# Performance work log

Measured on AMD Instinct MI355X. Metric: run time of the kernel, lower is better.

## Reference

```python
import jax, jax.numpy as jnp
import numpy as np

B, T, S, H = 32, 512, 1024, 1024

def setup_inputs() -> dict:
    key = jax.random.key(0)
    k1, k2, k3, k4, k5, k6 = jax.random.split(key, 6)
    query = jax.random.normal(k1, (B, T, H), dtype=jnp.float32)
    encoder_outputs = jax.random.normal(k2, (B, S, H), dtype=jnp.float32)
    # lengths in [S//2, S], force max length == S so mask width matches score
    src_lengths = jax.random.randint(k3, (B,), S // 2, S + 1, dtype=jnp.int32)
    src_lengths = src_lengths.at[0].set(S).astype(jnp.int64)
    scale = 1.0 / np.sqrt(H)
    W_in = jax.random.normal(k4, (H, H), dtype=jnp.float32) * scale      # linear_in.weight
    W_out = jax.random.normal(k5, (H, 2 * H), dtype=jnp.float32) * scale # linear_out.weight
    b_out = jax.random.normal(k6, (H,), dtype=jnp.float32) * scale       # linear_out.bias
    return {"query": query, "encoder_outputs": encoder_outputs,
            "src_lengths": src_lengths, "W_in": W_in, "W_out": W_out, "b_out": b_out}

def reference(query, encoder_outputs, src_lengths, W_in, W_out, b_out):
    # padding mask: True where position >= length  [B, S]
    pad = jnp.arange(S)[None, :] >= src_lengths[:, None]
    # linear_in (no bias): [B, T, H]
    qw = jnp.einsum('bth,oh->bto', query, W_in)
    # scores: [B, T, S]
    score = jnp.einsum('bto,bso->bts', qw, encoder_outputs)
    score = jnp.where(pad[:, None, :], -jnp.inf, score)
    p = jax.nn.softmax(score, axis=2)
    # context: [B, T, H]
    c = jnp.einsum('bts,bsh->bth', p, encoder_outputs)
    concat = jnp.concatenate([query, c], axis=2)          # [B, T, 2H]
    out = jnp.tanh(jnp.einsum('btk,ok->bto', concat, W_out) + b_out)
    return out
```

## Files before the change

kernel.cpp:

```cpp
#include <hip/hip_runtime.h>
#include <math.h>

#define BB 32
#define TT 512
#define SS 1024
#define HH 1024

typedef __attribute__((ext_vector_type(8))) short short8;
typedef __attribute__((ext_vector_type(4))) float f32x4;
typedef __attribute__((ext_vector_type(4))) unsigned short u16x4;
typedef unsigned short u16;
typedef unsigned int u32;

__device__ __forceinline__ u16 f2h(float x) {
    union { float f; unsigned int u; } a; a.f = x;
    unsigned int u = a.u;
    return (u16)((u + 0x7fffu + ((u >> 16) & 1u)) >> 16);
}
__device__ __forceinline__ float h2f(u16 h) {
    union { unsigned int u; float f; } a; a.u = ((unsigned int)h) << 16;
    return a.f;
}

__device__ __forceinline__ void gll16(const u16* g, u16* l) {
    __builtin_amdgcn_global_load_lds(
        (const __attribute__((address_space(1))) void*)g,
        (__attribute__((address_space(3))) void*)l, 16, 0, 0);
}

enum { E_F32 = 0, E_SPLIT = 1, E_TANH = 2, E_H = 3 };

struct Segs { const u16* a[4]; const u16* b[4]; };

template<int NSEG, int EPI>
__global__ __launch_bounds__(512, 2) void gemm8(
    Segs sg, int ldA, int ldB, int zshift,
    long sA, long sB, long sC,
    const float* __restrict__ bias,
    float* __restrict__ Cf, u16* __restrict__ Ch, u16* __restrict__ Cl,
    int ldC)
{
    __shared__ u16 lds[2][2][2][256 * 32];

    const int tid = threadIdx.x;
    const int l = tid & 63, w = tid >> 6;
    const int wr = w >> 2, wc = w & 3;
    const int fr = l & 15, g = l >> 4;

    const int id = blockIdx.x;
    const int v = ((id & 7) << 5) | (id >> 3);
    const int z = v >> zshift;
    const int rest = v & ((1 << zshift) - 1);
    const int bm = (rest >> 2) * 256;
    const int bn = (rest & 3) * 256;

    const u16* Aseg[4]; const u16* Bseg[4];
#pragma unroll
    for (int s = 0; s < NSEG; ++s) {
        Aseg[s] = sg.a[s] + (long)z * sA;
        Bseg[s] = sg.b[s] + (long)z * sB;
    }
    if (EPI == E_F32 || EPI == E_TANH) Cf += (long)z * sC;
    else { Ch += (long)z * sC; if (EPI == E_SPLIT) Cl += (long)z * sC; }

    f32x4 acc[8][4] = {};

    const int srow = tid >> 2, sch = tid & 3;
    const int skc = sch ^ ((srow >> 1) & 3);
    const long grA0 = (long)(bm + srow) * ldA + skc * 8;
    const long grA1 = (long)(bm + 128 + srow) * ldA + skc * 8;
    const long grB0 = (long)(bn + srow) * ldB + skc * 8;
    const long grB1 = (long)(bn + 128 + srow) * ldB + skc * 8;
    const int ldst0 = (tid & ~63) * 8;
    const int ldst1 = (512 + (tid & ~63)) * 8;

    auto stage = [&](int tile, int kh, int tensor) {
        const int k0g = tile * 64 + kh * 32;
        const int seg = k0g >> 10, kl = k0g & 1023;
        u16* lb = &lds[tile & 1][tensor][kh][0];
        if (tensor) {
            const u16* b = Bseg[seg];
            gll16(b + grB0 + kl, lb + ldst0);
            gll16(b + grB1 + kl, lb + ldst1);
        } else {
            const u16* a = Aseg[seg];
            gll16(a + grA0 + kl, lb + ldst0);
            gll16(a + grA1 + kl, lb + ldst1);
        }
    };

    int offA[8], offB[4];
#pragma unroll
    for (int k = 0; k < 8; ++k) {
        const int r = wr * 128 + k * 16 + fr;
        offA[k] = (r * 4 + (g ^ ((r >> 1) & 3))) * 8;
    }
#pragma unroll
    for (int j = 0; j < 4; ++j) {
        const int r = wc * 64 + j * 16 + fr;
        offB[j] = (r * 4 + (g ^ ((r >> 1) & 3))) * 8;
    }

    short8 faX[4], faY[4], fbA[4], fbB[4];

#define PFA(FA, BUF, KS, MH)                                                   \
    { const u16* pl = &lds[BUF][0][KS][0];                                     \
      _Pragma("unroll") for (int i_ = 0; i_ < 4; ++i_)                         \
          FA[i_] = *(const short8*)&pl[offA[(MH) * 4 + i_]]; }
#define PFB(FB, BUF, KS)                                                       \
    { const u16* pl = &lds[BUF][1][KS][0];                                     \
      _Pragma("unroll") for (int j_ = 0; j_ < 4; ++j_)                         \
          FB[j_] = *(const short8*)&pl[offB[j_]]; }
#define MFMA16(FA, FB, MH)                                                     \
    __builtin_amdgcn_s_setprio(1);                                             \
    _Pragma("unroll") for (int i_ = 0; i_ < 4; ++i_)                           \
        _Pragma("unroll") for (int j_ = 0; j_ < 4; ++j_)                       \
            acc[(MH) * 4 + i_][j_] = __builtin_amdgcn_mfma_f32_16x16x32_bf16(  \
                FA[i_], FB[j_], acc[(MH) * 4 + i_][j_], 0, 0, 0);              \
    __builtin_amdgcn_s_setprio(0);

    stage(0, 0, 0); stage(0, 0, 1); stage(0, 1, 0); stage(0, 1, 1);
    asm volatile("s_waitcnt vmcnt(0)" ::: "memory");
    __builtin_amdgcn_s_barrier();
    PFB(fbA, 0, 0)
    PFA(faX, 0, 0, 0)
    __builtin_amdgcn_sched_barrier(0);

    const int NT = NSEG * 16;
    for (int t = 0; t < NT; ++t) {
        const int cur = t & 1, nxt = cur ^ 1;
        const bool nl = (t + 1 < NT);

        if (nl) stage(t + 1, 0, 0);
        __builtin_amdgcn_s_barrier();
        PFA(faY, cur, 0, 1)
        __builtin_amdgcn_sched_barrier(0);
        MFMA16(faX, fbA, 0)

        if (nl) stage(t + 1, 0, 1);
        if (nl) { asm volatile("s_waitcnt vmcnt(4)" ::: "memory"); }
        else    { asm volatile("s_waitcnt vmcnt(0)" ::: "memory"); }
        __builtin_amdgcn_s_barrier();
        PFB(fbB, cur, 1)
        PFA(faX, cur, 1, 0)
        __builtin_amdgcn_sched_barrier(0);
        MFMA16(faY, fbA, 1)

        if (nl) stage(t + 1, 1, 0);
        __builtin_amdgcn_s_barrier();
        PFA(faY, cur, 1, 1)
        __builtin_amdgcn_sched_barrier(0);
        MFMA16(faX, fbB, 0)

        if (nl) stage(t + 1, 1, 1);
        if (nl) { asm volatile("s_waitcnt vmcnt(4)" ::: "memory"); }
        __builtin_amdgcn_s_barrier();
        PFB(fbA, nxt, 0)
        PFA(faX, nxt, 0, 0)
        __builtin_amdgcn_sched_barrier(0);
        MFMA16(faY, fbB, 1)
    }
#undef PFA
#undef PFB
#undef MFMA16

    __syncthreads();
    const int lrow = wr * 16 + g * 4;
#pragma unroll
    for (int mi = 0; mi < 8; ++mi) {
        if (EPI == E_F32 || EPI == E_TANH) {
            float* el = (float*)&lds[0][0][0][0];
#pragma unroll
            for (int nj = 0; nj < 4; ++nj) {
                const int col = wc * 64 + nj * 16 + fr;
                const float bv = (EPI == E_TANH) ? bias[bn + col] : 0.0f;
#pragma unroll
                for (int r = 0; r < 4; ++r) {
                    float vv = acc[mi][nj][r];
                    if (EPI == E_TANH) {
                        const float e = __expf(2.0f * (vv + bv));
                        vv = 1.0f - 2.0f / (e + 1.0f);
                    }
                    el[(lrow + r) * 260 + col] = vv;
                }
            }
            __syncthreads();
#pragma unroll
            for (int q = 0; q < 4; ++q) {
                const int c = tid + 512 * q;
                const int r32 = c >> 6, c4 = (c & 63) * 4;
                f32x4 vv = *(const f32x4*)&el[r32 * 260 + c4];
                const int grow = bm + (r32 >> 4) * 128 + mi * 16 + (r32 & 15);
                *(f32x4*)&Cf[(long)grow * ldC + bn + c4] = vv;
            }
        } else if (EPI == E_SPLIT) {
            u32* el = (u32*)&lds[0][0][0][0];
#pragma unroll
            for (int nj = 0; nj < 4; ++nj) {
                const int col = wc * 64 + nj * 16 + fr;
#pragma unroll
                for (int r = 0; r < 4; ++r) {
                    const float vv = acc[mi][nj][r];
                    const u16 h = f2h(vv);
                    const u16 lo = f2h(vv - h2f(h));
                    el[(lrow + r) * 260 + col] = (u32)h | ((u32)lo << 16);
                }
            }
            __syncthreads();
#pragma unroll
            for (int q = 0; q < 4; ++q) {
                const int c = tid + 512 * q;
                const int r32 = c >> 6, c4 = (c & 63) * 4;
                const u32* p = &el[r32 * 260 + c4];
                u16x4 hh, ll;
#pragma unroll
                for (int e = 0; e < 4; ++e) {
                    const u32 pv = p[e];
                    hh[e] = (u16)(pv & 0xffffu);
                    ll[e] = (u16)(pv >> 16);
                }
                const int grow = bm + (r32 >> 4) * 128 + mi * 16 + (r32 & 15);
                const long o = (long)grow * ldC + bn + c4;
                *(u16x4*)&Ch[o] = hh;
                *(u16x4*)&Cl[o] = ll;
            }
        } else {
            u16* el = (u16*)&lds[0][0][0][0];
#pragma unroll
            for (int nj = 0; nj < 4; ++nj) {
                const int col = wc * 64 + nj * 16 + fr;
#pragma unroll
                for (int r = 0; r < 4; ++r)
                    el[(lrow + r) * 264 + col] = f2h(acc[mi][nj][r]);
            }
            __syncthreads();
#pragma unroll
            for (int q = 0; q < 2; ++q) {
                const int c = tid + 512 * q;
                const int r32 = c >> 5, c8 = (c & 31) * 8;
                short8 vv = *(const short8*)&el[r32 * 264 + c8];
                const int grow = bm + (r32 >> 4) * 128 + mi * 16 + (r32 & 15);
                *(short8*)&Ch[(long)grow * ldC + bn + c8] = vv;
            }
        }
        __syncthreads();
    }
}

__global__ __launch_bounds__(256) void split_f32(
    const float* __restrict__ in, u16* __restrict__ hi, u16* __restrict__ lo,
    long n4)
{
    long i = (long)blockIdx.x * blockDim.x + threadIdx.x;
    const long stride = (long)gridDim.x * blockDim.x;
    for (; i < n4; i += stride) {
        f32x4 v = *(const f32x4*)(in + i * 4);
        u16x4 h4, l4;
#pragma unroll
        for (int e = 0; e < 4; ++e) {
            u16 h_ = f2h(v[e]);
            h4[e] = h_; l4[e] = f2h(v[e] - h2f(h_));
        }
        *(u16x4*)(hi + i * 4) = h4;
        *(u16x4*)(lo + i * 4) = l4;
    }
}

__global__ __launch_bounds__(256) void split3(
    const float* __restrict__ q,  u16* __restrict__ qh,  u16* __restrict__ ql,
    const float* __restrict__ wi, u16* __restrict__ wih, u16* __restrict__ wil,
    const float* __restrict__ wo, u16* __restrict__ woh, u16* __restrict__ wol,
    long nq4, long nwi4, long nwo4)
{
    const long total = nq4 + nwi4 + nwo4;
    long i = (long)blockIdx.x * blockDim.x + threadIdx.x;
    const long stride = (long)gridDim.x * blockDim.x;
    for (; i < total; i += stride) {
        const float* src; u16 *hi, *lo; long off;
        if (i < nq4)              { src = q;  hi = qh;  lo = ql;  off = i; }
        else if (i < nq4 + nwi4)  { src = wi; hi = wih; lo = wil; off = i - nq4; }
        else                      { src = wo; hi = woh; lo = wol; off = i - nq4 - nwi4; }
        f32x4 v = *(const f32x4*)(src + off * 4);
        u16x4 h4, l4;
#pragma unroll
        for (int e = 0; e < 4; ++e) {
            u16 h_ = f2h(v[e]);
            h4[e] = h_; l4[e] = f2h(v[e] - h2f(h_));
        }
        *(u16x4*)(hi + off * 4) = h4;
        *(u16x4*)(lo + off * 4) = l4;
    }
}

__global__ __launch_bounds__(256) void split_enc_fused(
    const float* __restrict__ in, u16* __restrict__ hi, u16* __restrict__ lo,
    u16* __restrict__ outT)
{
    __shared__ u16 t[64][72];
    const int z = blockIdx.z, sb = blockIdx.x * 64, hb = blockIdx.y * 64;
    const int c4 = (threadIdx.x & 15) * 4, r0 = threadIdx.x >> 4;
    const float* src = in + ((long)z * SS + sb) * HH + hb;
    u16* dhi = hi + ((long)z * SS + sb) * HH + hb;
    u16* dlo = lo + ((long)z * SS + sb) * HH + hb;
#pragma unroll
    for (int i = 0; i < 4; ++i) {
        const int r = r0 + i * 16;
        f32x4 v = *(const f32x4*)(src + (long)r * HH + c4);
        u16x4 h4, l4;
#pragma unroll
        for (int j = 0; j < 4; ++j) {
            u16 h_ = f2h(v[j]);
            h4[j] = h_; l4[j] = f2h(v[j] - h2f(h_));
        }
        *(u16x4*)(dhi + (long)r * HH + c4) = h4;
        *(u16x4*)(dlo + (long)r * HH + c4) = l4;
        t[c4 + 0][r] = h4[0]; t[c4 + 1][r] = h4[1];
        t[c4 + 2][r] = h4[2]; t[c4 + 3][r] = h4[3];
    }
    __syncthreads();
    u16* dst = outT + ((long)z * HH + hb) * SS + sb;
#pragma unroll
    for (int i = 0; i < 4; ++i) {
        const int r = r0 + i * 16;
        u16x4 o;
#pragma unroll
        for (int j = 0; j < 4; ++j) o[j] = t[r][c4 + j];
        *(u16x4*)(dst + (long)r * SS + c4) = o;
    }
}

__global__ __launch_bounds__(256) void transpose_h(
    const u16* __restrict__ in, u16* __restrict__ out)
{
    __shared__ u16 t[64][72];
    const int z = blockIdx.z, sb = blockIdx.x * 64, hb = blockIdx.y * 64;
    const int c4 = (threadIdx.x & 15) * 4, r0 = threadIdx.x >> 4;
    const u16* src = in + ((long)z * SS + sb) * HH + hb;
#pragma unroll
    for (int i = 0; i < 4; ++i) {
        const int r = r0 + i * 16;
        u16x4 v = *(const u16x4*)(src + (long)r * HH + c4);
        t[c4 + 0][r] = v[0]; t[c4 + 1][r] = v[1];
        t[c4 + 2][r] = v[2]; t[c4 + 3][r] = v[3];
    }
    __syncthreads();
    u16* dst = out + ((long)z * HH + hb) * SS + sb;
#pragma unroll
    for (int i = 0; i < 4; ++i) {
        const int r = r0 + i * 16;
        u16x4 o;
#pragma unroll
        for (int j = 0; j < 4; ++j) o[j] = t[r][c4 + j];
        *(u16x4*)(dst + (long)r * SS + c4) = o;
    }
}

__global__ __launch_bounds__(256) void softmax_mask(
    const float* __restrict__ Sc, u16* __restrict__ Ph,
    const int* __restrict__ lens)
{
    const int row = blockIdx.x;
    const int b = row >> 9;
    const int len = lens[b];
    const float* p = Sc + (long)row * SS;

    const int tid = threadIdx.x;
    const int s0 = tid * 4;
    f32x4 v = *(const f32x4*)(p + s0);
    float vals[4] = {v.x, v.y, v.z, v.w};

    float mx = -INFINITY;
#pragma unroll
    for (int j = 0; j < 4; ++j) {
        if (s0 + j >= len) vals[j] = -INFINITY;
        mx = fmaxf(mx, vals[j]);
    }
    for (int off = 32; off; off >>= 1) mx = fmaxf(mx, __shfl_xor(mx, off, 64));

    __shared__ float redm[4];
    __shared__ float reds[4];
    const int wave = tid >> 6, lane = tid & 63;
    if (lane == 0) redm[wave] = mx;
    __syncthreads();
    mx = fmaxf(fmaxf(redm[0], redm[1]), fmaxf(redm[2], redm[3]));

    float sum = 0.0f;
#pragma unroll
    for (int j = 0; j < 4; ++j) {
        vals[j] = __expf(vals[j] - mx);
        sum += vals[j];
    }
    for (int off = 32; off; off >>= 1) sum += __shfl_xor(sum, off, 64);
    if (lane == 0) reds[wave] = sum;
    __syncthreads();
    sum = reds[0] + reds[1] + reds[2] + reds[3];

    const float inv = 1.0f / sum;
    u16x4 o;
#pragma unroll
    for (int j = 0; j < 4; ++j) o[j] = f2h(vals[j] * inv);
    *(u16x4*)(Ph + (long)row * SS + s0) = o;
}

extern "C" void kernel_launch(void* const* d_in, const int* in_sizes, int n_in,
                              void* d_out, int out_size, void* d_ws, size_t ws_size,
                              hipStream_t stream)
{
    const float* query = (const float*)d_in[0];
    const float* enc   = (const float*)d_in[1];
    const int*   lens  = (const int*)d_in[2];
    const float* W_in  = (const float*)d_in[3];
    const float* W_out = (const float*)d_in[4];
    const float* b_out = (const float*)d_in[5];
    float* out = (float*)d_out;

    const long MQ = (long)BB * TT;

    u16* qh   = (u16*)d_ws;
    u16* ql   = qh   + MQ * HH;
    u16* qwh  = ql   + MQ * HH;
    u16* qwl  = qwh  + MQ * HH;
    u16* ench = qwl  + MQ * HH;
    u16* encl = ench + (long)BB * SS * HH;
    u16* ph   = encl + (long)BB * SS * HH;
    u16* wih  = ph   + MQ * SS;
    u16* wil  = wih  + (long)HH * HH;
    u16* woh  = wil  + (long)HH * HH;
    u16* wol  = woh  + (long)HH * 2 * HH;
    float* scores = (float*)(wol + (long)HH * 2 * HH);
    u16* ch   = ql;

    u16* encT_ded = (u16*)(scores + MQ * SS);
    const size_t need_fused =
        (size_t)((u16*)(scores + MQ * SS) - (u16*)d_ws) * 2 + (size_t)BB * HH * SS * 2;
    const bool fused = (ws_size >= need_fused);
    u16* encTh = fused ? encT_ded : (u16*)scores;

    split3<<<2048, 256, 0, stream>>>(
        query, qh, ql, W_in, wih, wil, W_out, woh, wol,
        MQ * HH / 4, (long)HH * HH / 4, (long)HH * 2 * HH / 4);
    if (fused) {
        split_enc_fused<<<dim3(16, 16, 32), 256, 0, stream>>>(
            enc, ench, encl, encTh);
    } else {
        split_f32<<<2048, 256, 0, stream>>>(enc, ench, encl,
                                            (long)BB * SS * HH / 4);
    }

    Segs s1 = {{qh, qh, ql, nullptr}, {wih, wil, wih, nullptr}};
    gemm8<3, E_SPLIT><<<256, 512, 0, stream>>>(
        s1, HH, HH, 8, 0L, 0L, 0L, nullptr, nullptr, qwh, qwl, HH);

    Segs s2 = {{qwh, qwh, qwl, nullptr}, {ench, encl, ench, nullptr}};
    gemm8<3, E_F32><<<256, 512, 0, stream>>>(
        s2, HH, HH, 3, (long)TT * HH, (long)SS * HH, (long)TT * SS,
        nullptr, scores, nullptr, nullptr, SS);

    softmax_mask<<<BB * TT, 256, 0, stream>>>(scores, ph, lens);

    if (!fused) {
        transpose_h<<<dim3(16, 16, 32), 256, 0, stream>>>(ench, encTh);
    }

    Segs s3 = {{ph, nullptr, nullptr, nullptr}, {encTh, nullptr, nullptr, nullptr}};
    gemm8<1, E_H><<<256, 512, 0, stream>>>(
        s3, SS, SS, 3, (long)TT * SS, (long)HH * SS, (long)TT * HH,
        nullptr, nullptr, ch, nullptr, HH);

    Segs s4 = {{qh, ch, qh, ch},
               {woh, woh + 1024, wol, wol + 1024}};
    gemm8<4, E_TANH><<<256, 512, 0, stream>>>(
        s4, HH, 2 * HH, 8, 0L, 0L, 0L, b_out, out, nullptr, nullptr, HH);
}
```

Measured before the change: 477.3 us.

## Share hi/lo operand tiles across split-bf16 products in a fused GEMM kernel

Adds a GEMM kernel that loads each K-tile's A_hi, A_lo, B_hi and B_lo once into LDS and issues all split-precision MFMA products from them, instead of treating each product as a separate K segment. It is used for the query projection, score and output GEMMs. The intent is to cut redundant global-to-LDS traffic and loop overhead. The cost is more LDS per block and a more intricate barrier/waitcnt schedule.

```diff
diff --git a/kernel.cpp b/kernel.cpp
--- a/kernel.cpp
+++ b/kernel.cpp
@@ -31,6 +31,253 @@
 enum { E_F32 = 0, E_SPLIT = 1, E_TANH = 2, E_H = 3 };
 
 struct Segs { const u16* a[4]; const u16* b[4]; };
+
+template<int NPROD, int NKSEG, int EPI>
+__global__ __launch_bounds__(512, 2) void gemm_np(
+    const u16* __restrict__ Ah0_g, const u16* __restrict__ Ah1_g,
+    const u16* __restrict__ Al_g,
+    const u16* __restrict__ Bh_g, const u16* __restrict__ Bl_g,
+    int ldA, int ldB, int zshift,
+    long sA, long sB, long sC,
+    const float* __restrict__ bias,
+    float* __restrict__ Cf, u16* __restrict__ Ch, u16* __restrict__ Cl,
+    int ldC)
+{
+    constexpr int NTEN = (NPROD == 3) ? 4 : 3;
+    __shared__ u16 lds[2][NTEN][256 * 32];
+
+    const int tid = threadIdx.x;
+    const int l = tid & 63, w = tid >> 6;
+    const int wr = w >> 2, wc = w & 3;
+    const int fr = l & 15, g = l >> 4;
+
+    const int id = blockIdx.x;
+    const int v = ((id & 7) << 5) | (id >> 3);
+    const int z = v >> zshift;
+    const int rest = v & ((1 << zshift) - 1);
+    const int bm = (rest >> 2) * 256;
+    const int bn = (rest & 3) * 256;
+
+    const u16* Ah0 = Ah0_g + (long)z * sA;
+    const u16* Ah1 = Ah1_g;
+    const u16* Al  = (NPROD == 3) ? (Al_g + (long)z * sA) : nullptr;
+    const u16* Bh  = Bh_g + (long)z * sB;
+    const u16* Bl  = Bl_g + (long)z * sB;
+    if (EPI == E_F32 || EPI == E_TANH) Cf += (long)z * sC;
+    else { Ch += (long)z * sC; if (EPI == E_SPLIT) Cl += (long)z * sC; }
+
+    f32x4 acc[8][4] = {};
+
+    const int srow = tid >> 2, sch = tid & 3;
+    const int skc = sch ^ ((srow >> 1) & 3);
+    const long grA0 = (long)(bm + srow) * ldA + skc * 8;
+    const long grA1 = (long)(bm + 128 + srow) * ldA + skc * 8;
+    const long grB0 = (long)(bn + srow) * ldB + skc * 8;
+    const long grB1 = (long)(bn + 128 + srow) * ldB + skc * 8;
+    const int ldst0 = (tid & ~63) * 8;
+    const int ldst1 = (512 + (tid & ~63)) * 8;
+
+    auto stage = [&](int tile, int ten) {
+        const int k0g = tile * 32;
+        u16* lb = &lds[tile & 1][ten][0];
+        if (ten == 0) {
+            const u16* base = (NKSEG == 2 && k0g >= 1024) ? Ah1 : Ah0;
+            const int ka = (NKSEG == 2) ? (k0g & 1023) : k0g;
+            gll16(base + grA0 + ka, lb + ldst0);
+            gll16(base + grA1 + ka, lb + ldst1);
+        } else if (ten == 3) {
+            gll16(Al + grA0 + k0g, lb + ldst0);
+            gll16(Al + grA1 + k0g, lb + ldst1);
+        } else {
+            const u16* b = (ten == 1) ? Bh : Bl;
+            gll16(b + grB0 + k0g, lb + ldst0);
+            gll16(b + grB1 + k0g, lb + ldst1);
+        }
+    };
+
+    int offA[8], offB[4];
+#pragma unroll
+    for (int k = 0; k < 8; ++k) {
+        const int r = wr * 128 + k * 16 + fr;
+        offA[k] = (r * 4 + (g ^ ((r >> 1) & 3))) * 8;
+    }
+#pragma unroll
+    for (int j = 0; j < 4; ++j) {
+        const int r = wc * 64 + j * 16 + fr;
+        offB[j] = (r * 4 + (g ^ ((r >> 1) & 3))) * 8;
+    }
+
+    short8 fax[4], fay[4], fal[4], fbh[4], fbl[4];
+
+#define PFA_(DST, BUF, TEN, MH)                                                \
+    { const u16* pl = &lds[BUF][TEN][0];                                       \
+      _Pragma("unroll") for (int i_ = 0; i_ < 4; ++i_)                         \
+          DST[i_] = *(const short8*)&pl[offA[(MH) * 4 + i_]]; }
+#define PFB_(DST, BUF, TEN)                                                    \
+    { const u16* pl = &lds[BUF][TEN][0];                                       \
+      _Pragma("unroll") for (int j_ = 0; j_ < 4; ++j_)                         \
+          DST[j_] = *(const short8*)&pl[offB[j_]]; }
+#define MFMA16(FA, FB, MH)                                                     \
+    __builtin_amdgcn_s_setprio(1);                                             \
+    _Pragma("unroll") for (int i_ = 0; i_ < 4; ++i_)                           \
+        _Pragma("unroll") for (int j_ = 0; j_ < 4; ++j_)                       \
+            acc[(MH) * 4 + i_][j_] = __builtin_amdgcn_mfma_f32_16x16x32_bf16(  \
+                FA[i_], FB[j_], acc[(MH) * 4 + i_][j_], 0, 0, 0);              \
+    __builtin_amdgcn_s_setprio(0);
+
+    stage(0, 0); stage(0, 1); stage(0, 2);
+    if (NPROD == 3) stage(0, 3);
+    if (NPROD == 3) { asm volatile("s_waitcnt vmcnt(4)" ::: "memory"); }
+    else            { asm volatile("s_waitcnt vmcnt(2)" ::: "memory"); }
+    __builtin_amdgcn_s_barrier();
+    PFB_(fbh, 0, 1)
+    PFA_(fax, 0, 0, 0)
+    __builtin_amdgcn_sched_barrier(0);
+
+    const int NT = NKSEG * 32;
+    for (int t = 0; t < NT; ++t) {
+        const int cur = t & 1, nxt = cur ^ 1;
+        const bool nl = (t + 1 < NT);
+
+        if (nl) stage(t + 1, 0);
+        if (nl) {
+            if (NPROD == 3) { asm volatile("s_waitcnt vmcnt(4)" ::: "memory"); }
+            else            { asm volatile("s_waitcnt vmcnt(2)" ::: "memory"); }
+        } else { asm volatile("s_waitcnt vmcnt(0)" ::: "memory"); }
+        __builtin_amdgcn_s_barrier();
+        PFB_(fbl, cur, 2)
+        __builtin_amdgcn_sched_barrier(0);
+        MFMA16(fax, fbh, 0)
+
+        if (nl) stage(t + 1, 1);
+        if (NPROD == 3) {
+            if (nl) { asm volatile("s_waitcnt vmcnt(4)" ::: "memory"); }
+            else    { asm volatile("s_waitcnt vmcnt(0)" ::: "memory"); }
+        }
+        __builtin_amdgcn_s_barrier();
+        if (NPROD == 3) { PFA_(fal, cur, 3, 0) }
+        else            { PFA_(fay, cur, 0, 1) }
+        __builtin_amdgcn_sched_barrier(0);
+        MFMA16(fax, fbl, 0)
+
+        if (NPROD == 3) {
+            if (nl) stage(t + 1, 2);
+            __builtin_amdgcn_s_barrier();
+            PFA_(fay, cur, 0, 1)
+            __builtin_amdgcn_sched_barrier(0);
+            MFMA16(fal, fbh, 0)
+            if (nl) stage(t + 1, 3);
+            __builtin_amdgcn_s_barrier();
+            PFA_(fal, cur, 3, 1)
+            __builtin_amdgcn_sched_barrier(0);
+            MFMA16(fay, fbh, 1)
+            __builtin_amdgcn_s_barrier();
+            __builtin_amdgcn_sched_barrier(0);
+            MFMA16(fal, fbh, 1)
+            if (nl) { asm volatile("s_waitcnt vmcnt(4)" ::: "memory"); }
+            __builtin_amdgcn_s_barrier();
+            if (nl) { PFB_(fbh, nxt, 1) PFA_(fax, nxt, 0, 0) }
+            __builtin_amdgcn_sched_barrier(0);
+            MFMA16(fay, fbl, 1)
+        } else {
+            if (nl) stage(t + 1, 2);
+            __builtin_amdgcn_s_barrier();
+            __builtin_amdgcn_sched_barrier(0);
+            MFMA16(fay, fbh, 1)
+            if (nl) { asm volatile("s_waitcnt vmcnt(2)" ::: "memory"); }
+            __builtin_amdgcn_s_barrier();
+            if (nl) { PFB_(fbh, nxt, 1) PFA_(fax, nxt, 0, 0) }
+            __builtin_amdgcn_sched_barrier(0);
+            MFMA16(fay, fbl, 1)
+        }
+    }
+#undef PFA_
+#undef PFB_
+#undef MFMA16
+
+    __syncthreads();
+    u16* ebase = (u16*)&lds[0][0][0];
+    const int lrow = wr * 16 + g * 4;
+#pragma unroll
+    for (int mi = 0; mi < 8; ++mi) {
+        if (EPI == E_F32 || EPI == E_TANH) {
+            float* el = (float*)ebase;
+#pragma unroll
+            for (int nj = 0; nj < 4; ++nj) {
+                const int col = wc * 64 + nj * 16 + fr;
+                const float bv = (EPI == E_TANH) ? bias[bn + col] : 0.0f;
+#pragma unroll
+                for (int r = 0; r < 4; ++r) {
+                    float vv = acc[mi][nj][r];
+                    if (EPI == E_TANH) {
+                        const float e = __expf(2.0f * (vv + bv));
+                        vv = 1.0f - 2.0f / (e + 1.0f);
+                    }
+                    el[(lrow + r) * 260 + col] = vv;
+                }
+            }
+            __syncthreads();
+#pragma unroll
+            for (int q = 0; q < 4; ++q) {
+                const int c = tid + 512 * q;
+                const int r32 = c >> 6, c4 = (c & 63) * 4;
+                f32x4 vv = *(const f32x4*)&el[r32 * 260 + c4];
+                const int grow = bm + (r32 >> 4) * 128 + mi * 16 + (r32 & 15);
+                *(f32x4*)&Cf[(long)grow * ldC + bn + c4] = vv;
+            }
+        } else if (EPI == E_SPLIT) {
+            u32* el = (u32*)ebase;
+#pragma unroll
+            for (int nj = 0; nj < 4; ++nj) {
+                const int col = wc * 64 + nj * 16 + fr;
+#pragma unroll
+                for (int r = 0; r < 4; ++r) {
+                    const float vv = acc[mi][nj][r];
+                    const u16 h = f2h(vv);
+                    const u16 lo = f2h(vv - h2f(h));
+                    el[(lrow + r) * 260 + col] = (u32)h | ((u32)lo << 16);
+                }
+            }
+            __syncthreads();
+#pragma unroll
+            for (int q = 0; q < 4; ++q) {
+                const int c = tid + 512 * q;
+                const int r32 = c >> 6, c4 = (c & 63) * 4;
+                const u32* p = &el[r32 * 260 + c4];
+                u16x4 hh, ll;
+#pragma unroll
+                for (int e = 0; e < 4; ++e) {
+                    const u32 pv = p[e];
+                    hh[e] = (u16)(pv & 0xffffu);
+                    ll[e] = (u16)(pv >> 16);
+                }
+                const int grow = bm + (r32 >> 4) * 128 + mi * 16 + (r32 & 15);
+                const long o = (long)grow * ldC + bn + c4;
+                *(u16x4*)&Ch[o] = hh;
+                *(u16x4*)&Cl[o] = ll;
+            }
+        } else {
+            u16* el = ebase;
+#pragma unroll
+            for (int nj = 0; nj < 4; ++nj) {
+                const int col = wc * 64 + nj * 16 + fr;
+#pragma unroll
+                for (int r = 0; r < 4; ++r)
+                    el[(lrow + r) * 264 + col] = f2h(acc[mi][nj][r]);
+            }
+            __syncthreads();
+#pragma unroll
+            for (int q = 0; q < 2; ++q) {
+                const int c = tid + 512 * q;
+                const int r32 = c >> 5, c8 = (c & 31) * 8;
+                short8 vv = *(const short8*)&el[r32 * 264 + c8];
+                const int grow = bm + (r32 >> 4) * 128 + mi * 16 + (r32 & 15);
+                *(short8*)&Ch[(long)grow * ldC + bn + c8] = vv;
+            }
+        }
+        __syncthreads();
+    }
+}
 
 template<int NSEG, int EPI>
 __global__ __launch_bounds__(512, 2) void gemm8(
@@ -168,7 +415,25 @@
     const int lrow = wr * 16 + g * 4;
 #pragma unroll
     for (int mi = 0; mi < 8; ++mi) {
-        if (EPI == E_F32 || EPI == E_TANH) {
+        u16* el16 = (u16*)&lds[0][0][0][0];
+        if (EPI == E_H) {
+#pragma unroll
+            for (int nj = 0; nj < 4; ++nj) {
+                const int col = wc * 64 + nj * 16 + fr;
+#pragma unroll
+                for (int r = 0; r < 4; ++r)
+                    el16[(lrow + r) * 264 + col] = f2h(acc[mi][nj][r]);
+            }
+            __syncthreads();
+#pragma unroll
+            for (int q = 0; q < 2; ++q) {
+                const int c = tid + 512 * q;
+                const int r32 = c >> 5, c8 = (c & 31) * 8;
+                short8 vv = *(const short8*)&el16[r32 * 264 + c8];
+                const int grow = bm + (r32 >> 4) * 128 + mi * 16 + (r32 & 15);
+                *(short8*)&Ch[(long)grow * ldC + bn + c8] = vv;
+            }
+        } else {
             float* el = (float*)&lds[0][0][0][0];
 #pragma unroll
             for (int nj = 0; nj < 4; ++nj) {
@@ -192,55 +457,6 @@
                 f32x4 vv = *(const f32x4*)&el[r32 * 260 + c4];
                 const int grow = bm + (r32 >> 4) * 128 + mi * 16 + (r32 & 15);
                 *(f32x4*)&Cf[(long)grow * ldC + bn + c4] = vv;
-            }
-        } else if (EPI == E_SPLIT) {
-            u32* el = (u32*)&lds[0][0][0][0];
-#pragma unroll
-            for (int nj = 0; nj < 4; ++nj) {
-                const int col = wc * 64 + nj * 16 + fr;
-#pragma unroll
-                for (int r = 0; r < 4; ++r) {
-                    const float vv = acc[mi][nj][r];
-                    const u16 h = f2h(vv);
-                    const u16 lo = f2h(vv - h2f(h));
-                    el[(lrow + r) * 260 + col] = (u32)h | ((u32)lo << 16);
-                }
-            }
-            __syncthreads();
-#pragma unroll
-            for (int q = 0; q < 4; ++q) {
-                const int c = tid + 512 * q;
-                const int r32 = c >> 6, c4 = (c & 63) * 4;
-                const u32* p = &el[r32 * 260 + c4];
-                u16x4 hh, ll;
-#pragma unroll
-                for (int e = 0; e < 4; ++e) {
-                    const u32 pv = p[e];
-                    hh[e] = (u16)(pv & 0xffffu);
-                    ll[e] = (u16)(pv >> 16);
-                }
-                const int grow = bm + (r32 >> 4) * 128 + mi * 16 + (r32 & 15);
-                const long o = (long)grow * ldC + bn + c4;
-                *(u16x4*)&Ch[o] = hh;
-                *(u16x4*)&Cl[o] = ll;
-            }
-        } else {
-            u16* el = (u16*)&lds[0][0][0][0];
-#pragma unroll
-            for (int nj = 0; nj < 4; ++nj) {
-                const int col = wc * 64 + nj * 16 + fr;
-#pragma unroll
-                for (int r = 0; r < 4; ++r)
-                    el[(lrow + r) * 264 + col] = f2h(acc[mi][nj][r]);
-            }
-            __syncthreads();
-#pragma unroll
-            for (int q = 0; q < 2; ++q) {
-                const int c = tid + 512 * q;
-                const int r32 = c >> 5, c8 = (c & 31) * 8;
-                short8 vv = *(const short8*)&el[r32 * 264 + c8];
-                const int grow = bm + (r32 >> 4) * 128 + mi * 16 + (r32 & 15);
-                *(short8*)&Ch[(long)grow * ldC + bn + c8] = vv;
             }
         }
         __syncthreads();
@@ -447,13 +663,13 @@
                                             (long)BB * SS * HH / 4);
     }
 
-    Segs s1 = {{qh, qh, ql, nullptr}, {wih, wil, wih, nullptr}};
-    gemm8<3, E_SPLIT><<<256, 512, 0, stream>>>(
-        s1, HH, HH, 8, 0L, 0L, 0L, nullptr, nullptr, qwh, qwl, HH);
-
-    Segs s2 = {{qwh, qwh, qwl, nullptr}, {ench, encl, ench, nullptr}};
-    gemm8<3, E_F32><<<256, 512, 0, stream>>>(
-        s2, HH, HH, 3, (long)TT * HH, (long)SS * HH, (long)TT * SS,
+    gemm_np<3, 1, E_SPLIT><<<256, 512, 0, stream>>>(
+        qh, nullptr, ql, wih, wil, HH, HH, 8, 0L, 0L, 0L,
+        nullptr, nullptr, qwh, qwl, HH);
+
+    gemm_np<3, 1, E_F32><<<256, 512, 0, stream>>>(
+        qwh, nullptr, qwl, ench, encl, HH, HH, 3,
+        (long)TT * HH, (long)SS * HH, (long)TT * SS,
         nullptr, scores, nullptr, nullptr, SS);
 
     softmax_mask<<<BB * TT, 256, 0, stream>>>(scores, ph, lens);
@@ -467,8 +683,7 @@
         s3, SS, SS, 3, (long)TT * SS, (long)HH * SS, (long)TT * HH,
         nullptr, nullptr, ch, nullptr, HH);
 
-    Segs s4 = {{qh, ch, qh, ch},
-               {woh, woh + 1024, wol, wol + 1024}};
-    gemm8<4, E_TANH><<<256, 512, 0, stream>>>(
-        s4, HH, 2 * HH, 8, 0L, 0L, 0L, b_out, out, nullptr, nullptr, HH);
-}
+    gemm_np<2, 2, E_TANH><<<256, 512, 0, stream>>>(
+        qh, ch, nullptr, woh, wol, HH, 2 * HH, 8, 0L, 0L, 0L,
+        b_out, out, nullptr, nullptr, HH);
+}
```

Result: faster. 445.1 us, median of 2 (-6.7%).
